# Kernel tuning notes

Hardware: AMD Instinct MI355X
Metric: run time of the kernel (lower is better)

## Reference

```python
import jax, jax.numpy as jnp
import numpy as np

N = 50000      # nodes
E = 800000     # edges (avg degree 16)
D = 512        # in_features
H = 512        # gcn hidden dim (both layers)
G = 64         # graphs in batch
C = 10         # num_classes


def setup_inputs() -> dict:
    key = jax.random.key(0)
    ks = jax.random.split(key, 12)
    x = jax.random.normal(ks[0], (N, D), dtype=jnp.float32)
    edge_index = jax.random.randint(ks[1], (2, E), 0, N, dtype=jnp.int64)
    batch = jnp.sort(jax.random.randint(ks[2], (N,), 0, G, dtype=jnp.int64))
    w = lambda k, sh: (jax.random.normal(k, sh, dtype=jnp.float32) * 0.02)
    return {
        "x": x,
        "edge_index": edge_index,
        "batch": batch,
        # GraphConv layer 0: lin_rel (weight+bias) applied to aggregated neighbors,
        # lin_root (weight, no bias) applied to self features.
        "Wr0": w(ks[3], (D, H)), "br0": jnp.zeros((H,), jnp.float32), "Ws0": w(ks[4], (D, H)),
        # GraphConv layer 1
        "Wr1": w(ks[5], (H, H)), "br1": jnp.zeros((H,), jnp.float32), "Ws1": w(ks[6], (H, H)),
        # final Linear
        "Wl": w(ks[7], (H, C)), "bl": jnp.zeros((C,), jnp.float32),
    }


def _graph_conv(x, src, dst, Wr, br, Ws):
    # sum-aggregate neighbor features: agg[i] = sum_{(j->i) in E} x[j]
    agg = jax.ops.segment_sum(x[src], dst, num_segments=N)  # [N, d_in]
    return agg @ Wr + br + x @ Ws                           # [N, d_out]


def reference(x, edge_index, batch, Wr0, br0, Ws0, Wr1, br1, Ws1, Wl, bl):
    src, dst = edge_index[0], edge_index[1]
    h = jax.nn.relu(_graph_conv(x, src, dst, Wr0, br0, Ws0))   # dropout = identity (eval)
    h = jax.nn.relu(_graph_conv(h, src, dst, Wr1, br1, Ws1))
    # global mean pool over graphs
    sums = jax.ops.segment_sum(h, batch, num_segments=G)                       # [G, H]
    counts = jax.ops.segment_sum(jnp.ones((N, 1), h.dtype), batch, num_segments=G)
    pooled = jax.nn.relu(sums / jnp.maximum(counts, 1.0))
    return pooled @ Wl + bl  # [G, C]
```

## Files before the change

### kernel.cpp

```cpp
#include <hip/hip_runtime.h>

#define NN 50000
#define NE 800000
#define MP 50048
#define GG 64
#define HD 512
#define K2 1024
#define SCAN_BLKS 196

typedef __attribute__((ext_vector_type(8))) short bf16x8;
typedef __attribute__((ext_vector_type(4))) float f32x4;

__device__ __forceinline__ unsigned short f2bf(float f) {
  unsigned u = __builtin_bit_cast(unsigned, f);
  u += 0x7fffu + ((u >> 16) & 1u);
  return (unsigned short)(u >> 16);
}
__device__ __forceinline__ float bf2f(unsigned short h) {
  unsigned u = ((unsigned)h) << 16;
  return __builtin_bit_cast(float, u);
}

__device__ __forceinline__ void g2l16(const void* g, void* l) {
  __builtin_amdgcn_global_load_lds(
      (const __attribute__((address_space(1))) unsigned int*)g,
      (__attribute__((address_space(3))) unsigned int*)l, 16, 0, 0);
}

__global__ void wt_kernel(const float* __restrict__ Wr, const float* __restrict__ Ws,
                          unsigned short* __restrict__ Wt) {
  int idx = blockIdx.x * 256 + threadIdx.x;
  if (idx >= HD * K2) return;
  int n = idx >> 10;
  int k = idx & (K2 - 1);
  float v = (k < HD) ? Wr[k * HD + n] : Ws[(k - HD) * HD + n];
  Wt[idx] = f2bf(v);
}

__global__ void cvtpad_kernel(const float* __restrict__ in, unsigned short* __restrict__ out,
                              int rows_in, long long total4) {
  long long i = (long long)blockIdx.x * 256 + threadIdx.x;
  for (; i < total4; i += (long long)gridDim.x * 256) {
    int r = (int)((i * 4) >> 9);
    float4 v = make_float4(0.f, 0.f, 0.f, 0.f);
    if (r < rows_in) v = ((const float4*)in)[i];
    ushort4 o;
    o.x = f2bf(v.x); o.y = f2bf(v.y); o.z = f2bf(v.z); o.w = f2bf(v.w);
    ((ushort4*)out)[i] = o;
  }
}

__global__ void hist_kernel(const int* __restrict__ ei, int* __restrict__ deg) {
  int i = blockIdx.x * 256 + threadIdx.x;
  if (i < NE) atomicAdd(&deg[ei[NE + i]], 1);
}

__global__ __launch_bounds__(256) void scan1_kernel(const int* __restrict__ deg,
                                                    int* __restrict__ tmp,
                                                    int* __restrict__ bsum) {
  __shared__ int sh[256];
  int t = threadIdx.x;
  int i = blockIdx.x * 256 + t;
  int v = (i < NN) ? deg[i] : 0;
  sh[t] = v;
  __syncthreads();
#pragma unroll
  for (int off = 1; off < 256; off <<= 1) {
    int u = (t >= off) ? sh[t - off] : 0;
    __syncthreads();
    sh[t] += u;
    __syncthreads();
  }
  if (i < NN) tmp[i] = sh[t] - v;
  if (t == 255) bsum[blockIdx.x] = sh[255];
}

__global__ __launch_bounds__(256) void scan2_kernel(int* __restrict__ bsum,
                                                    int* __restrict__ row_ptr) {
  __shared__ int sh[256];
  int t = threadIdx.x;
  int v = (t < SCAN_BLKS) ? bsum[t] : 0;
  sh[t] = v;
  __syncthreads();
#pragma unroll
  for (int off = 1; off < 256; off <<= 1) {
    int u = (t >= off) ? sh[t - off] : 0;
    __syncthreads();
    sh[t] += u;
    __syncthreads();
  }
  if (t < SCAN_BLKS) bsum[t] = sh[t] - v;
  if (t == 255) row_ptr[NN] = sh[255];
}

__global__ __launch_bounds__(256) void scan3_kernel(const int* __restrict__ tmp,
                                                    const int* __restrict__ bsum,
                                                    int* __restrict__ row_ptr,
                                                    int* __restrict__ cursor) {
  int i = blockIdx.x * 256 + threadIdx.x;
  if (i < NN) {
    int r = tmp[i] + bsum[blockIdx.x];
    row_ptr[i] = r;
    cursor[i] = r;
  }
}

__global__ void fill_kernel(const int* __restrict__ ei, int* __restrict__ cursor,
                            int* __restrict__ col) {
  int i = blockIdx.x * 256 + threadIdx.x;
  if (i < NE) {
    int d = ei[NE + i];
    int p = atomicAdd(&cursor[d], 1);
    col[p] = ei[i];
  }
}

__global__ __launch_bounds__(256) void gather_kernel(const unsigned short* __restrict__ X,
                                                     const int* __restrict__ row_ptr,
                                                     const int* __restrict__ col,
                                                     unsigned short* __restrict__ out) {
  int w = (blockIdx.x * 256 + threadIdx.x) >> 6;
  int lane = threadIdx.x & 63;
  if (w >= MP) return;
  float a0 = 0.f, a1 = 0.f, a2 = 0.f, a3 = 0.f, a4 = 0.f, a5 = 0.f, a6 = 0.f, a7 = 0.f;
  if (w < NN) {
    int r0 = row_ptr[w], r1 = row_ptr[w + 1];
    for (int base = r0; base < r1; base += 64) {
      int idx = base + lane;
      int myc = (idx < r1) ? col[idx] : 0;
      int cnt = min(64, r1 - base);
      #pragma unroll 8
      for (int j = 0; j < cnt; j++) {
        int c = __shfl(myc, j);
        uint4 v = *(const uint4*)(X + (size_t)c * HD + lane * 8);
        a0 += bf2f((unsigned short)(v.x & 0xffff));
        a1 += bf2f((unsigned short)(v.x >> 16));
        a2 += bf2f((unsigned short)(v.y & 0xffff));
        a3 += bf2f((unsigned short)(v.y >> 16));
        a4 += bf2f((unsigned short)(v.z & 0xffff));
        a5 += bf2f((unsigned short)(v.z >> 16));
        a6 += bf2f((unsigned short)(v.w & 0xffff));
        a7 += bf2f((unsigned short)(v.w >> 16));
      }
    }
  }
  uint4 o;
  o.x = ((unsigned)f2bf(a1) << 16) | f2bf(a0);
  o.y = ((unsigned)f2bf(a3) << 16) | f2bf(a2);
  o.z = ((unsigned)f2bf(a5) << 16) | f2bf(a4);
  o.w = ((unsigned)f2bf(a7) << 16) | f2bf(a6);
  *(uint4*)(out + (size_t)w * HD + lane * 8) = o;
}

__global__ __launch_bounds__(512, 2) void gemm_kernel(
    const unsigned short* __restrict__ A0, const unsigned short* __restrict__ A1,
    const unsigned short* __restrict__ Wt, const float* __restrict__ bias,
    unsigned short* __restrict__ Hout) {
  __shared__ __align__(16) unsigned short Ads[128 * 64];
  __shared__ __align__(16) unsigned short Bds[256 * 64];

  const int tid = threadIdx.x;
  const int lane = tid & 63;
  const int wv = tid >> 6;
  const int wm = wv >> 2;
  const int wn = wv & 3;

  const int nwg = 782;
  const int orig = blockIdx.x;
  const int q = nwg >> 3, r8 = nwg & 7;
  const int xcd = orig & 7;
  const int wgid = (xcd < r8 ? xcd * (q + 1) : r8 * (q + 1) + (xcd - r8) * q) + (orig >> 3);

  const int mt = wgid >> 1;
  const int nt = wgid & 1;
  const int row0 = mt * 128;
  const int col0 = nt * 256;

  f32x4 acc[4][4];
#pragma unroll
  for (int i = 0; i < 4; i++)
#pragma unroll
    for (int j = 0; j < 4; j++) acc[i][j] = (f32x4)(0.f);

  const int lr = lane >> 3;
  const int lc = lane & 7;
  const int csw = lc ^ lr;

  for (int kt = 0; kt < 16; ++kt) {
    const int k0 = kt * 64;
    const unsigned short* Asrc = (k0 < HD) ? A0 : A1;
    const int ka = k0 & (HD - 1);
#pragma unroll
    for (int it = 0; it < 2; ++it) {
      int rg = it * 8 + wv;
      g2l16(Asrc + (size_t)(row0 + rg * 8 + lr) * HD + ka + csw * 8, &Ads[rg * 8 * 64]);
    }
#pragma unroll
    for (int it = 0; it < 4; ++it) {
      int rg = it * 8 + wv;
      g2l16(Wt + (size_t)(col0 + rg * 8 + lr) * K2 + k0 + csw * 8, &Bds[rg * 8 * 64]);
    }
    __syncthreads();
#pragma unroll
    for (int kk = 0; kk < 2; ++kk) {
      bf16x8 af[4], bfr[4];
#pragma unroll
      for (int m = 0; m < 4; m++) {
        int r = wm * 64 + m * 16 + (lane & 15);
        int ck = (kk * 4 + (lane >> 4)) ^ (r & 7);
        af[m] = *(const bf16x8*)&Ads[r * 64 + ck * 8];
      }
#pragma unroll
      for (int n = 0; n < 4; n++) {
        int r = wn * 64 + n * 16 + (lane & 15);
        int ck = (kk * 4 + (lane >> 4)) ^ (r & 7);
        bfr[n] = *(const bf16x8*)&Bds[r * 64 + ck * 8];
      }
#pragma unroll
      for (int m = 0; m < 4; m++)
#pragma unroll
        for (int n = 0; n < 4; n++)
          acc[m][n] = __builtin_amdgcn_mfma_f32_16x16x32_bf16(af[m], bfr[n], acc[m][n], 0, 0, 0);
    }
    __syncthreads();
  }

#pragma unroll
  for (int n = 0; n < 4; n++) {
    int c = col0 + wn * 64 + n * 16 + (lane & 15);
    float bv = bias[c];
#pragma unroll
    for (int m = 0; m < 4; m++) {
      int rbase = row0 + wm * 64 + m * 16 + (lane >> 4) * 4;
#pragma unroll
      for (int r = 0; r < 4; r++) {
        float v = acc[m][n][r] + bv;
        v = v > 0.f ? v : 0.f;
        Hout[(size_t)(rbase + r) * HD + c] = f2bf(v);
      }
    }
  }
}

__device__ __forceinline__ int lbound(const int* b, int v) {
  int lo = 0, hi = NN;
  while (lo < hi) { int m = (lo + hi) >> 1; if (b[m] < v) lo = m + 1; else hi = m; }
  return lo;
}

__global__ void pool_kernel(const unsigned short* __restrict__ H, const int* __restrict__ batch,
                            float* __restrict__ pooled) {
  int b = blockIdx.x;
  int g = b >> 4;
  int half = (b >> 3) & 1;
  int chunk = b & 7;
  int col = half * 256 + threadIdx.x;
  int start = lbound(batch, g);
  int end = lbound(batch, g + 1);
  int len = end - start;
  int r0 = start + (int)(((long long)len * chunk) >> 3);
  int r1 = start + (int)(((long long)len * (chunk + 1)) >> 3);
  float s = 0.f;
  for (int r = r0; r < r1; r++) s += bf2f(H[(size_t)r * HD + col]);
  atomicAdd(&pooled[g * HD + col], s);
}

__global__ void final_kernel(const float* __restrict__ pooled, const int* __restrict__ batch,
                             const float* __restrict__ Wl, const float* __restrict__ bl,
                             float* __restrict__ out) {
  int g = blockIdx.x;
  int t = threadIdx.x;
  int lane = t & 63, wv = t >> 6;
  int start = lbound(batch, g);
  int end = lbound(batch, g + 1);
  float cnt = (float)(end - start);
  if (cnt < 1.f) cnt = 1.f;
  float a[10];
#pragma unroll
  for (int c = 0; c < 10; c++) a[c] = 0.f;
  for (int n = t; n < HD; n += 256) {
    float p = pooled[g * HD + n] / cnt;
    p = p > 0.f ? p : 0.f;
#pragma unroll
    for (int c = 0; c < 10; c++) a[c] += p * Wl[n * 10 + c];
  }
  __shared__ float red[10][4];
#pragma unroll
  for (int c = 0; c < 10; c++) {
    float v = a[c];
#pragma unroll
    for (int off = 32; off >= 1; off >>= 1) v += __shfl_down(v, off);
    if (lane == 0) red[c][wv] = v;
  }
  __syncthreads();
  if (t < 10) out[g * 10 + t] = red[t][0] + red[t][1] + red[t][2] + red[t][3] + bl[t];
}

extern "C" void kernel_launch(void* const* d_in, const int* in_sizes, int n_in,
                              void* d_out, int out_size, void* d_ws, size_t ws_size,
                              hipStream_t stream) {
  const float* x   = (const float*)d_in[0];
  const int* ei    = (const int*)d_in[1];
  const int* batch = (const int*)d_in[2];
  const float* Wr0 = (const float*)d_in[3];
  const float* br0 = (const float*)d_in[4];
  const float* Ws0 = (const float*)d_in[5];
  const float* Wr1 = (const float*)d_in[6];
  const float* br1 = (const float*)d_in[7];
  const float* Ws1 = (const float*)d_in[8];
  const float* Wl  = (const float*)d_in[9];
  const float* bl  = (const float*)d_in[10];
  float* out = (float*)d_out;

  char* ws = (char*)d_ws;
  size_t off = 0;
  auto alloc = [&](size_t bytes) { char* p = ws + off; off += (bytes + 255) & ~255ULL; return p; };
  unsigned short* xb   = (unsigned short*)alloc((size_t)MP * HD * 2);
  unsigned short* h0   = (unsigned short*)alloc((size_t)MP * HD * 2);
  unsigned short* aggb = (unsigned short*)alloc((size_t)MP * HD * 2);
  unsigned short* Wt0  = (unsigned short*)alloc((size_t)HD * K2 * 2);
  unsigned short* Wt1  = (unsigned short*)alloc((size_t)HD * K2 * 2);
  float* pooled        = (float*)alloc((size_t)GG * HD * 4);
  int* deg             = (int*)alloc((size_t)NN * 4);
  int* row_ptr         = (int*)alloc((size_t)(NN + 1) * 4);
  int* cursor          = (int*)alloc((size_t)NN * 4);
  int* col             = (int*)alloc((size_t)NE * 4);
  int* stmp            = (int*)alloc((size_t)NN * 4);
  int* bsum            = (int*)alloc((size_t)256 * 4);
  unsigned short* h1 = xb;

  const long long totMP4 = (long long)MP * HD / 4;

  hipMemsetAsync(deg, 0, (size_t)NN * 4, stream);
  hist_kernel<<<(NE + 255) / 256, 256, 0, stream>>>(ei, deg);
  scan1_kernel<<<SCAN_BLKS, 256, 0, stream>>>(deg, stmp, bsum);
  scan2_kernel<<<1, 256, 0, stream>>>(bsum, row_ptr);
  scan3_kernel<<<SCAN_BLKS, 256, 0, stream>>>(stmp, bsum, row_ptr, cursor);
  fill_kernel<<<(NE + 255) / 256, 256, 0, stream>>>(ei, cursor, col);

  wt_kernel<<<2048, 256, 0, stream>>>(Wr0, Ws0, Wt0);
  wt_kernel<<<2048, 256, 0, stream>>>(Wr1, Ws1, Wt1);
  cvtpad_kernel<<<2048, 256, 0, stream>>>(x, xb, NN, totMP4);

  gather_kernel<<<MP / 4, 256, 0, stream>>>(xb, row_ptr, col, aggb);
  gemm_kernel<<<391 * 2, 512, 0, stream>>>(aggb, xb, Wt0, br0, h0);

  gather_kernel<<<MP / 4, 256, 0, stream>>>(h0, row_ptr, col, aggb);
  gemm_kernel<<<391 * 2, 512, 0, stream>>>(aggb, h0, Wt1, br1, h1);

  hipMemsetAsync(pooled, 0, (size_t)GG * HD * 4, stream);
  pool_kernel<<<GG * 16, 256, 0, stream>>>(h1, batch, pooled);
  final_kernel<<<GG, 256, 0, stream>>>(pooled, batch, Wl, bl, out);
}
```

Measured before the change: 667.6 us.

## Fuse prep kernels, gather two rows per wave, double-buffer full-width GEMM

Three preparation kernels (weight transpose, x conversion, degree histogram) become one launch, and the weight transpose now goes through shared memory so its reads are coalesced. The gather kernel handles two destination rows per wave to keep more independent loads in flight. The GEMM switches to a 64x512 tile that reads the whole N dimension, so A is loaded once, and double-buffers the LDS loads to overlap them with MFMA. The price is LDS use of about 144KB per block, which limits occupancy, and some divergence in the gather when the two rows have different degrees.

```diff
diff --git a/kernel.cpp b/kernel.cpp
--- a/kernel.cpp
+++ b/kernel.cpp
@@ -27,32 +27,49 @@
       (__attribute__((address_space(3))) unsigned int*)l, 16, 0, 0);
 }
 
-__global__ void wt_kernel(const float* __restrict__ Wr, const float* __restrict__ Ws,
-                          unsigned short* __restrict__ Wt) {
-  int idx = blockIdx.x * 256 + threadIdx.x;
-  if (idx >= HD * K2) return;
-  int n = idx >> 10;
-  int k = idx & (K2 - 1);
-  float v = (k < HD) ? Wr[k * HD + n] : Ws[(k - HD) * HD + n];
-  Wt[idx] = f2bf(v);
-}
-
-__global__ void cvtpad_kernel(const float* __restrict__ in, unsigned short* __restrict__ out,
-                              int rows_in, long long total4) {
-  long long i = (long long)blockIdx.x * 256 + threadIdx.x;
-  for (; i < total4; i += (long long)gridDim.x * 256) {
-    int r = (int)((i * 4) >> 9);
-    float4 v = make_float4(0.f, 0.f, 0.f, 0.f);
-    if (r < rows_in) v = ((const float4*)in)[i];
-    ushort4 o;
-    o.x = f2bf(v.x); o.y = f2bf(v.y); o.z = f2bf(v.z); o.w = f2bf(v.w);
-    ((ushort4*)out)[i] = o;
-  }
-}
-
-__global__ void hist_kernel(const int* __restrict__ ei, int* __restrict__ deg) {
-  int i = blockIdx.x * 256 + threadIdx.x;
-  if (i < NE) atomicAdd(&deg[ei[NE + i]], 1);
+__global__ __launch_bounds__(256) void prep_kernel(
+    const float* __restrict__ x, unsigned short* __restrict__ xb,
+    const float* __restrict__ Wr0, const float* __restrict__ Ws0, unsigned short* __restrict__ Wt0,
+    const float* __restrict__ Wr1, const float* __restrict__ Ws1, unsigned short* __restrict__ Wt1,
+    const int* __restrict__ ei, int* __restrict__ deg) {
+  int b = blockIdx.x, t = threadIdx.x;
+  if (b < 256) {
+    __shared__ float sh[64][65];
+    int layer = b >> 7, tl = b & 127;
+    int tn = tl >> 4, tk = tl & 15;
+    int half = tk >> 3;
+    int kw = (tk & 7) * 64, n0 = tn * 64;
+    const float* W = layer ? (half ? Ws1 : Wr1) : (half ? Ws0 : Wr0);
+    unsigned short* Wt = layer ? Wt1 : Wt0;
+    int nn = t & 63;
+    int kb = t >> 6;
+#pragma unroll
+    for (int i = 0; i < 16; i++) {
+      int kk = kb + i * 4;
+      sh[kk][nn] = W[(size_t)(kw + kk) * HD + n0 + nn];
+    }
+    __syncthreads();
+    int kk2 = t & 63;
+#pragma unroll
+    for (int i = 0; i < 16; i++) {
+      int nn2 = kb + i * 4;
+      Wt[(size_t)(n0 + nn2) * K2 + half * HD + kw + kk2] = f2bf(sh[kk2][nn2]);
+    }
+  } else if (b < 2304) {
+    const long long total4 = (long long)MP * HD / 4;
+    for (long long i = (long long)(b - 256) * 256 + t; i < total4; i += 2048LL * 256) {
+      int r = (int)((i * 4) >> 9);
+      float4 v = make_float4(0.f, 0.f, 0.f, 0.f);
+      if (r < NN) v = ((const float4*)x)[i];
+      ushort4 o;
+      o.x = f2bf(v.x); o.y = f2bf(v.y); o.z = f2bf(v.z); o.w = f2bf(v.w);
+      ((ushort4*)xb)[i] = o;
+    }
+  } else {
+    for (int i = (b - 2304) * 256 + t; i < NE; i += 512 * 256) {
+      atomicAdd(&deg[ei[NE + i]], 1);
+    }
+  }
 }
 
 __global__ __launch_bounds__(256) void scan1_kernel(const int* __restrict__ deg,
@@ -115,66 +132,81 @@
   }
 }
 
+#define ACC8(v, a)                                        \
+  a[0] += bf2f((unsigned short)((v).x & 0xffff));         \
+  a[1] += bf2f((unsigned short)((v).x >> 16));            \
+  a[2] += bf2f((unsigned short)((v).y & 0xffff));         \
+  a[3] += bf2f((unsigned short)((v).y >> 16));            \
+  a[4] += bf2f((unsigned short)((v).z & 0xffff));         \
+  a[5] += bf2f((unsigned short)((v).z >> 16));            \
+  a[6] += bf2f((unsigned short)((v).w & 0xffff));         \
+  a[7] += bf2f((unsigned short)((v).w >> 16));
+
 __global__ __launch_bounds__(256) void gather_kernel(const unsigned short* __restrict__ X,
                                                      const int* __restrict__ row_ptr,
                                                      const int* __restrict__ col,
                                                      unsigned short* __restrict__ out) {
-  int w = (blockIdx.x * 256 + threadIdx.x) >> 6;
+  int wid = (blockIdx.x * 256 + threadIdx.x) >> 6;
   int lane = threadIdx.x & 63;
-  if (w >= MP) return;
-  float a0 = 0.f, a1 = 0.f, a2 = 0.f, a3 = 0.f, a4 = 0.f, a5 = 0.f, a6 = 0.f, a7 = 0.f;
-  if (w < NN) {
-    int r0 = row_ptr[w], r1 = row_ptr[w + 1];
-    for (int base = r0; base < r1; base += 64) {
-      int idx = base + lane;
-      int myc = (idx < r1) ? col[idx] : 0;
-      int cnt = min(64, r1 - base);
-      #pragma unroll 8
-      for (int j = 0; j < cnt; j++) {
-        int c = __shfl(myc, j);
+  int rowA = wid * 2, rowB = wid * 2 + 1;
+  if (rowA >= MP) return;
+  float aA[8] = {0.f, 0.f, 0.f, 0.f, 0.f, 0.f, 0.f, 0.f};
+  float aB[8] = {0.f, 0.f, 0.f, 0.f, 0.f, 0.f, 0.f, 0.f};
+  int r0a = 0, r1a = 0, r0b = 0, r1b = 0;
+  if (rowA < NN) { r0a = row_ptr[rowA]; r1a = row_ptr[rowA + 1]; }
+  if (rowB < NN) { r0b = row_ptr[rowB]; r1b = row_ptr[rowB + 1]; }
+  int baseA = r0a, baseB = r0b;
+  while (baseA < r1a || baseB < r1b) {
+    int cntA = r1a - baseA; cntA = cntA < 0 ? 0 : (cntA > 64 ? 64 : cntA);
+    int cntB = r1b - baseB; cntB = cntB < 0 ? 0 : (cntB > 64 ? 64 : cntB);
+    int mycA = (lane < cntA) ? col[baseA + lane] : 0;
+    int mycB = (lane < cntB) ? col[baseB + lane] : 0;
+    int n = cntA > cntB ? cntA : cntB;
+#pragma unroll 4
+    for (int j = 0; j < n; j++) {
+      if (j < cntA) {
+        int c = __shfl(mycA, j);
         uint4 v = *(const uint4*)(X + (size_t)c * HD + lane * 8);
-        a0 += bf2f((unsigned short)(v.x & 0xffff));
-        a1 += bf2f((unsigned short)(v.x >> 16));
-        a2 += bf2f((unsigned short)(v.y & 0xffff));
-        a3 += bf2f((unsigned short)(v.y >> 16));
-        a4 += bf2f((unsigned short)(v.z & 0xffff));
-        a5 += bf2f((unsigned short)(v.z >> 16));
-        a6 += bf2f((unsigned short)(v.w & 0xffff));
-        a7 += bf2f((unsigned short)(v.w >> 16));
-      }
-    }
-  }
-  uint4 o;
-  o.x = ((unsigned)f2bf(a1) << 16) | f2bf(a0);
-  o.y = ((unsigned)f2bf(a3) << 16) | f2bf(a2);
-  o.z = ((unsigned)f2bf(a5) << 16) | f2bf(a4);
-  o.w = ((unsigned)f2bf(a7) << 16) | f2bf(a6);
-  *(uint4*)(out + (size_t)w * HD + lane * 8) = o;
+        ACC8(v, aA)
+      }
+      if (j < cntB) {
+        int c = __shfl(mycB, j);
+        uint4 v = *(const uint4*)(X + (size_t)c * HD + lane * 8);
+        ACC8(v, aB)
+      }
+    }
+    baseA += 64; baseB += 64;
+  }
+  uint4 oA, oB;
+  oA.x = ((unsigned)f2bf(aA[1]) << 16) | f2bf(aA[0]);
+  oA.y = ((unsigned)f2bf(aA[3]) << 16) | f2bf(aA[2]);
+  oA.z = ((unsigned)f2bf(aA[5]) << 16) | f2bf(aA[4]);
+  oA.w = ((unsigned)f2bf(aA[7]) << 16) | f2bf(aA[6]);
+  oB.x = ((unsigned)f2bf(aB[1]) << 16) | f2bf(aB[0]);
+  oB.y = ((unsigned)f2bf(aB[3]) << 16) | f2bf(aB[2]);
+  oB.z = ((unsigned)f2bf(aB[5]) << 16) | f2bf(aB[4]);
+  oB.w = ((unsigned)f2bf(aB[7]) << 16) | f2bf(aB[6]);
+  *(uint4*)(out + (size_t)rowA * HD + lane * 8) = oA;
+  *(uint4*)(out + (size_t)rowB * HD + lane * 8) = oB;
 }
 
 __global__ __launch_bounds__(512, 2) void gemm_kernel(
     const unsigned short* __restrict__ A0, const unsigned short* __restrict__ A1,
     const unsigned short* __restrict__ Wt, const float* __restrict__ bias,
     unsigned short* __restrict__ Hout) {
-  __shared__ __align__(16) unsigned short Ads[128 * 64];
-  __shared__ __align__(16) unsigned short Bds[256 * 64];
+  __shared__ __align__(16) unsigned short Ads[2][64 * 64];
+  __shared__ __align__(16) unsigned short Bds[2][512 * 64];
 
   const int tid = threadIdx.x;
   const int lane = tid & 63;
   const int wv = tid >> 6;
-  const int wm = wv >> 2;
-  const int wn = wv & 3;
 
   const int nwg = 782;
   const int orig = blockIdx.x;
   const int q = nwg >> 3, r8 = nwg & 7;
   const int xcd = orig & 7;
-  const int wgid = (xcd < r8 ? xcd * (q + 1) : r8 * (q + 1) + (xcd - r8) * q) + (orig >> 3);
-
-  const int mt = wgid >> 1;
-  const int nt = wgid & 1;
-  const int row0 = mt * 128;
-  const int col0 = nt * 256;
+  const int mt = (xcd < r8 ? xcd * (q + 1) : r8 * (q + 1) + (xcd - r8) * q) + (orig >> 3);
+  const int row0 = mt * 64;
 
   f32x4 acc[4][4];
 #pragma unroll
@@ -182,39 +214,43 @@
 #pragma unroll
     for (int j = 0; j < 4; j++) acc[i][j] = (f32x4)(0.f);
 
-  const int lr = lane >> 3;
-  const int lc = lane & 7;
-  const int csw = lc ^ lr;
+  const int sr = tid >> 3;
+  const int sc = tid & 7;
+  const int csw = sc ^ (sr & 7);
+
+  int cur = 0;
+  {
+    g2l16(A0 + (size_t)(row0 + sr) * HD + csw * 8, &Ads[0][tid * 8]);
+#pragma unroll
+    for (int it = 0; it < 8; it++)
+      g2l16(Wt + (size_t)(it * 64 + sr) * K2 + csw * 8, &Bds[0][it * 4096 + tid * 8]);
+  }
+  __syncthreads();
 
   for (int kt = 0; kt < 16; ++kt) {
-    const int k0 = kt * 64;
-    const unsigned short* Asrc = (k0 < HD) ? A0 : A1;
-    const int ka = k0 & (HD - 1);
-#pragma unroll
-    for (int it = 0; it < 2; ++it) {
-      int rg = it * 8 + wv;
-      g2l16(Asrc + (size_t)(row0 + rg * 8 + lr) * HD + ka + csw * 8, &Ads[rg * 8 * 64]);
-    }
-#pragma unroll
-    for (int it = 0; it < 4; ++it) {
-      int rg = it * 8 + wv;
-      g2l16(Wt + (size_t)(col0 + rg * 8 + lr) * K2 + k0 + csw * 8, &Bds[rg * 8 * 64]);
-    }
-    __syncthreads();
+    if (kt < 15) {
+      const int k0 = (kt + 1) * 64;
+      const unsigned short* Asrc = (k0 < HD) ? A0 : A1;
+      const int ka = k0 & (HD - 1);
+      g2l16(Asrc + (size_t)(row0 + sr) * HD + ka + csw * 8, &Ads[cur ^ 1][tid * 8]);
+#pragma unroll
+      for (int it = 0; it < 8; it++)
+        g2l16(Wt + (size_t)(it * 64 + sr) * K2 + k0 + csw * 8, &Bds[cur ^ 1][it * 4096 + tid * 8]);
+    }
 #pragma unroll
     for (int kk = 0; kk < 2; ++kk) {
       bf16x8 af[4], bfr[4];
 #pragma unroll
       for (int m = 0; m < 4; m++) {
-        int r = wm * 64 + m * 16 + (lane & 15);
+        int r = m * 16 + (lane & 15);
         int ck = (kk * 4 + (lane >> 4)) ^ (r & 7);
-        af[m] = *(const bf16x8*)&Ads[r * 64 + ck * 8];
+        af[m] = *(const bf16x8*)&Ads[cur][r * 64 + ck * 8];
       }
 #pragma unroll
       for (int n = 0; n < 4; n++) {
-        int r = wn * 64 + n * 16 + (lane & 15);
+        int r = wv * 64 + n * 16 + (lane & 15);
         int ck = (kk * 4 + (lane >> 4)) ^ (r & 7);
-        bfr[n] = *(const bf16x8*)&Bds[r * 64 + ck * 8];
+        bfr[n] = *(const bf16x8*)&Bds[cur][r * 64 + ck * 8];
       }
 #pragma unroll
       for (int m = 0; m < 4; m++)
@@ -223,15 +259,16 @@
           acc[m][n] = __builtin_amdgcn_mfma_f32_16x16x32_bf16(af[m], bfr[n], acc[m][n], 0, 0, 0);
     }
     __syncthreads();
+    cur ^= 1;
   }
 
 #pragma unroll
   for (int n = 0; n < 4; n++) {
-    int c = col0 + wn * 64 + n * 16 + (lane & 15);
+    int c = wv * 64 + n * 16 + (lane & 15);
     float bv = bias[c];
 #pragma unroll
     for (int m = 0; m < 4; m++) {
-      int rbase = row0 + wm * 64 + m * 16 + (lane >> 4) * 4;
+      int rbase = row0 + m * 16 + (lane >> 4) * 4;
 #pragma unroll
       for (int r = 0; r < 4; r++) {
         float v = acc[m][n][r] + bv;
@@ -329,26 +366,22 @@
   int* bsum            = (int*)alloc((size_t)256 * 4);
   unsigned short* h1 = xb;
 
-  const long long totMP4 = (long long)MP * HD / 4;
-
   hipMemsetAsync(deg, 0, (size_t)NN * 4, stream);
-  hist_kernel<<<(NE + 255) / 256, 256, 0, stream>>>(ei, deg);
+  hipMemsetAsync(pooled, 0, (size_t)GG * HD * 4, stream);
+
+  prep_kernel<<<2816, 256, 0, stream>>>(x, xb, Wr0, Ws0, Wt0, Wr1, Ws1, Wt1, ei, deg);
+
   scan1_kernel<<<SCAN_BLKS, 256, 0, stream>>>(deg, stmp, bsum);
   scan2_kernel<<<1, 256, 0, stream>>>(bsum, row_ptr);
   scan3_kernel<<<SCAN_BLKS, 256, 0, stream>>>(stmp, bsum, row_ptr, cursor);
   fill_kernel<<<(NE + 255) / 256, 256, 0, stream>>>(ei, cursor, col);
 
-  wt_kernel<<<2048, 256, 0, stream>>>(Wr0, Ws0, Wt0);
-  wt_kernel<<<2048, 256, 0, stream>>>(Wr1, Ws1, Wt1);
-  cvtpad_kernel<<<2048, 256, 0, stream>>>(x, xb, NN, totMP4);
-
-  gather_kernel<<<MP / 4, 256, 0, stream>>>(xb, row_ptr, col, aggb);
-  gemm_kernel<<<391 * 2, 512, 0, stream>>>(aggb, xb, Wt0, br0, h0);
-
-  gather_kernel<<<MP / 4, 256, 0, stream>>>(h0, row_ptr, col, aggb);
-  gemm_kernel<<<391 * 2, 512, 0, stream>>>(aggb, h0, Wt1, br1, h1);
-
-  hipMemsetAsync(pooled, 0, (size_t)GG * HD * 4, stream);
+  gather_kernel<<<(MP / 2) / 4, 256, 0, stream>>>(xb, row_ptr, col, aggb);
+  gemm_kernel<<<782, 512, 0, stream>>>(aggb, xb, Wt0, br0, h0);
+
+  gather_kernel<<<(MP / 2) / 4, 256, 0, stream>>>(h0, row_ptr, col, aggb);
+  gemm_kernel<<<782, 512, 0, stream>>>(aggb, h0, Wt1, br1, h1);
+
   pool_kernel<<<GG * 16, 256, 0, stream>>>(h1, batch, pooled);
   final_kernel<<<GG, 256, 0, stream>>>(pooled, batch, Wl, bl, out);
 }
```

Measured after the change: 756.6 us. 13.3% more time.
